# Kernel tuning notes

Hardware: AMD Instinct MI355X
Metric: run time of the kernel (lower is better)

Reference implementation:

```python
import jax, jax.numpy as jnp
import numpy as np

N_NODES = 100000
N_EDGES = 800000
IN_DIM, HID_DIM, OUT_DIM = 128, 256, 128


def setup_inputs() -> dict:
    key = jax.random.key(0)
    ks = jax.random.split(key, 8)
    x = jax.random.normal(ks[0], (N_NODES, IN_DIM), dtype=jnp.float32)
    edge_index = jax.random.randint(ks[1], (2, N_EDGES), 0, N_NODES, dtype=jnp.int32)
    s = lambda k, shp, fan_in: jax.random.normal(k, shp, dtype=jnp.float32) / np.sqrt(fan_in)
    return {
        "x": x,
        "edge_index": edge_index,
        "W1_l": s(ks[2], (HID_DIM, IN_DIM), IN_DIM),   # applied to aggregated neighbors
        "b1": jnp.zeros((HID_DIM,), jnp.float32),
        "W1_r": s(ks[3], (HID_DIM, IN_DIM), IN_DIM),   # root/self transform (no bias, as in PyG)
        "W2_l": s(ks[4], (OUT_DIM, HID_DIM), HID_DIM),
        "b2": jnp.zeros((OUT_DIM,), jnp.float32),
        "W2_r": s(ks[5], (OUT_DIM, HID_DIM), HID_DIM),
    }


def _sage_conv(x, src, dst, W_l, b, W_r):
    # mean aggregation of source-neighbor features onto targets
    msg = x[src]                                              # [E, d]
    agg = jax.ops.segment_sum(msg, dst, num_segments=N_NODES)  # [N, d]
    cnt = jax.ops.segment_sum(jnp.ones((src.shape[0],), x.dtype), dst, num_segments=N_NODES)
    mean = agg / jnp.maximum(cnt, 1.0)[:, None]
    # SAGEConv: lin_l(aggr) + lin_r(x)
    return mean @ W_l.T + b + x @ W_r.T


def reference(x, edge_index, W1_l, b1, W1_r, W2_l, b2, W2_r):
    src, dst = edge_index[0], edge_index[1]
    h = jax.nn.relu(_sage_conv(x, src, dst, W1_l, b1, W1_r))
    # dropout p=0.0 -> identity (eval-mode equivalent)
    out = _sage_conv(h, src, dst, W2_l, b2, W2_r)
    return out
```

## Files before the change

### kernel.cpp

```cpp
#include <hip/hip_runtime.h>

#define NN 100000
#define NE 800000

typedef __attribute__((ext_vector_type(4))) float f32x4;
typedef __attribute__((ext_vector_type(4))) int   i32x4;
typedef __attribute__((ext_vector_type(8))) unsigned short u16x8;

__device__ __forceinline__ unsigned short f2bf(float f) {
  unsigned u = __float_as_uint(f);
  return (unsigned short)((u + 0x7FFFu + ((u >> 16) & 1u)) >> 16);
}
__device__ __forceinline__ float bf2f(unsigned short b) {
  return __uint_as_float(((unsigned)b) << 16);
}

__global__ void degree_k(const int* __restrict__ dst, int* __restrict__ deg,
                         int* __restrict__ rord) {
  int e = blockIdx.x * 256 + threadIdx.x;
  if (e < NE) rord[e] = atomicAdd(&deg[dst[e]], 1);
}

__global__ __launch_bounds__(256) void scan1_k(const int* __restrict__ deg,
    int* __restrict__ offs, int* __restrict__ bsum, float* __restrict__ inv) {
  __shared__ int s[256];
  int t = threadIdx.x;
  int base = blockIdx.x * 1024 + t * 4;
  int v[4], tsum = 0;
#pragma unroll
  for (int k = 0; k < 4; ++k) {
    int i = base + k;
    v[k] = (i < NN) ? deg[i] : 0;
    tsum += v[k];
    if (i < NN) inv[i] = 1.0f / fmaxf((float)v[k], 1.0f);
  }
  s[t] = tsum; __syncthreads();
  int val = tsum;
#pragma unroll
  for (int off = 1; off < 256; off <<= 1) {
    int x = (t >= off) ? s[t - off] : 0;
    __syncthreads();
    val += x; s[t] = val;
    __syncthreads();
  }
  int excl = val - tsum;
  if (t == 255) bsum[blockIdx.x] = val;
  int run = excl;
#pragma unroll
  for (int k = 0; k < 4; ++k) { int i = base + k; if (i < NN) offs[i] = run; run += v[k]; }
}

__global__ __launch_bounds__(256) void scan2_k(int* __restrict__ bsum, int nb) {
  __shared__ int s[256];
  int t = threadIdx.x;
  int v = (t < nb) ? bsum[t] : 0;
  s[t] = v; __syncthreads();
  int val = v;
#pragma unroll
  for (int off = 1; off < 256; off <<= 1) {
    int x = (t >= off) ? s[t - off] : 0;
    __syncthreads();
    val += x; s[t] = val;
    __syncthreads();
  }
  if (t < nb) bsum[t] = val - v;
}

__global__ __launch_bounds__(256) void scan3_k(int* __restrict__ offs,
    const int* __restrict__ bsum) {
  int base = blockIdx.x * 1024 + threadIdx.x * 4;
  int add = bsum[blockIdx.x];
#pragma unroll
  for (int k = 0; k < 4; ++k) {
    int i = base + k;
    if (i < NN) offs[i] += add;
  }
}

__global__ void fill_k(const int* __restrict__ src, const int* __restrict__ dst,
    const int* __restrict__ offs, const int* __restrict__ rord,
    int* __restrict__ eidx) {
  int e = blockIdx.x * 256 + threadIdx.x;
  if (e < NE) {
    int p = offs[dst[e]] + rord[e];
    __builtin_nontemporal_store(src[e], &eidx[p]);
  }
}

__global__ __launch_bounds__(256) void cast_x_k(const float* __restrict__ in,
    unsigned short* __restrict__ outb) {
  int i = blockIdx.x * 256 + threadIdx.x;
  if (i >= NN * 128 / 4) return;
  float4 v = *reinterpret_cast<const float4*>(in + (size_t)i * 4);
  ushort4 o;
  o.x = f2bf(v.x); o.y = f2bf(v.y); o.z = f2bf(v.z); o.w = f2bf(v.w);
  *reinterpret_cast<ushort4*>(outb + (size_t)i * 4) = o;
}

__global__ __launch_bounds__(256) void cast_w4_k(const float* __restrict__ Wa,
    const float* __restrict__ Wb, const float* __restrict__ Wc,
    const float* __restrict__ Wd, unsigned short* __restrict__ outb) {
  int i = blockIdx.x * 256 + threadIdx.x;
  if (i >= 4 * 32768) return;
  int seg = i >> 15, off = i & 32767;
  const float* s = (seg < 2) ? (seg == 0 ? Wa : Wb) : (seg == 2 ? Wc : Wd);
  outb[i] = f2bf(s[off]);
}

template<bool ACC>
__global__ __launch_bounds__(256) void gather_k(const unsigned short* __restrict__ feat,
    const int* __restrict__ offs, const int* __restrict__ deg,
    const float* __restrict__ inv, const int* __restrict__ eidx,
    unsigned short* __restrict__ outb, float* __restrict__ outf) {
  int node = blockIdx.x * 16 + (threadIdx.x >> 4);
  int l = threadIdx.x & 15;
  if (node >= NN) return;
  int st = offs[node], n = deg[node];
  float a[8];
#pragma unroll
  for (int k = 0; k < 8; ++k) a[k] = 0.f;

  int j = 0;
  for (; j + 4 <= n; j += 4) {
    int s0 = eidx[st + j + 0];
    int s1 = eidx[st + j + 1];
    int s2 = eidx[st + j + 2];
    int s3 = eidx[st + j + 3];
    u16x8 r0 = *reinterpret_cast<const u16x8*>(feat + (size_t)s0 * 128 + l * 8);
    u16x8 r1 = *reinterpret_cast<const u16x8*>(feat + (size_t)s1 * 128 + l * 8);
    u16x8 r2 = *reinterpret_cast<const u16x8*>(feat + (size_t)s2 * 128 + l * 8);
    u16x8 r3 = *reinterpret_cast<const u16x8*>(feat + (size_t)s3 * 128 + l * 8);
#pragma unroll
    for (int k = 0; k < 8; ++k)
      a[k] += (bf2f(r0[k]) + bf2f(r1[k])) + (bf2f(r2[k]) + bf2f(r3[k]));
  }
  for (; j < n; ++j) {
    int s = eidx[st + j];
    u16x8 r = *reinterpret_cast<const u16x8*>(feat + (size_t)s * 128 + l * 8);
#pragma unroll
    for (int k = 0; k < 8; ++k) a[k] += bf2f(r[k]);
  }

  float sc = inv[node];
  if (ACC) {
    float* po = outf + (size_t)node * 128 + l * 8;
    float4 o0 = *reinterpret_cast<const float4*>(po);
    float4 o1 = *reinterpret_cast<const float4*>(po + 4);
    o0.x += sc * a[0]; o0.y += sc * a[1]; o0.z += sc * a[2]; o0.w += sc * a[3];
    o1.x += sc * a[4]; o1.y += sc * a[5]; o1.z += sc * a[6]; o1.w += sc * a[7];
    *reinterpret_cast<float4*>(po) = o0;
    *reinterpret_cast<float4*>(po + 4) = o1;
  } else {
    u16x8 o;
#pragma unroll
    for (int k = 0; k < 8; ++k) o[k] = f2bf(sc * a[k]);
    *reinterpret_cast<u16x8*>(outb + (size_t)node * 128 + l * 8) = o;
  }
}

template<int MODE>
__global__ __launch_bounds__(256) void mgemm_k(
    const unsigned short* __restrict__ A1, const unsigned short* __restrict__ A2,
    const unsigned short* __restrict__ Wbase, const float* __restrict__ bias,
    unsigned short* __restrict__ outb, float* __restrict__ outf) {
  __shared__ unsigned short As[64 * 256];
  const int t = threadIdx.x;
  const int wave = t >> 6, lane = t & 63;
  const int lhi = lane >> 4, llo = lane & 15;
  const int row0 = blockIdx.x * 64;

#pragma unroll
  for (int c = 0; c < 8; ++c) {
    int chunk = wave * 8 + c;
    int tb = chunk * 1024 + lane * 16;
    int r = tb >> 9;
    int cb = tb & 511;
    int cbs = cb ^ ((r & 7) << 4);
    int gr = min(row0 + r, NN - 1);
    const char* gsrc;
    if (MODE == 0) {
      const unsigned short* Asel = (cbs < 256) ? A1 : A2;
      gsrc = (const char*)(Asel + (size_t)gr * 128) + (cbs & 255);
    } else {
      gsrc = (const char*)(A1 + (size_t)gr * 256) + cbs;
    }
    __builtin_amdgcn_global_load_lds(
        (const __attribute__((address_space(1))) void*)gsrc,
        (__attribute__((address_space(3))) void*)((char*)As + chunk * 1024),
        16, 0, 0);
  }

  const unsigned short* bp[4];
  float bv[4];
#pragma unroll
  for (int fn = 0; fn < 4; ++fn) {
    int c = wave * 64 + fn * 16 + llo;
    if (MODE == 0) {
      bp[fn] = Wbase + (size_t)c * 128;
      bv[fn] = bias[c];
    } else {
      bp[fn] = Wbase + (wave >= 2 ? 32768 : 0) + (size_t)(c & 127) * 256;
      bv[fn] = (wave >= 2) ? bias[c & 127] : 0.f;
    }
  }

  f32x4 acc[4][4];
#pragma unroll
  for (int fm = 0; fm < 4; ++fm)
#pragma unroll
    for (int fn = 0; fn < 4; ++fn) acc[fm][fn] = (f32x4)0.f;

  __syncthreads();

#pragma unroll 1
  for (int ks = 0; ks < 8; ++ks) {
    i32x4 a[4], b[4];
#pragma unroll
    for (int fm = 0; fm < 4; ++fm) {
      int r = fm * 16 + llo;
      int cb = (ks * 64 + lhi * 16) ^ ((r & 7) << 4);
      a[fm] = *reinterpret_cast<const i32x4*>((const char*)As + r * 512 + cb);
    }
    int koff = (MODE == 0) ? ((ks & 3) * 32 + lhi * 8 + ((ks >= 4) ? 32768 : 0))
                           : (ks * 32 + lhi * 8);
#pragma unroll
    for (int fn = 0; fn < 4; ++fn)
      b[fn] = *reinterpret_cast<const i32x4*>(bp[fn] + koff);
#pragma unroll
    for (int fm = 0; fm < 4; ++fm)
#pragma unroll
      for (int fn = 0; fn < 4; ++fn)
        asm("v_mfma_f32_16x16x32_bf16 %0, %1, %2, %0"
            : "+v"(acc[fm][fn]) : "v"(a[fm]), "v"(b[fn]));
  }

  asm volatile("s_nop 7\n\ts_nop 7");

#pragma unroll
  for (int fm = 0; fm < 4; ++fm) {
#pragma unroll
    for (int fn = 0; fn < 4; ++fn) {
      int col = wave * 64 + fn * 16 + llo;
#pragma unroll
      for (int j = 0; j < 4; ++j) {
        int row = row0 + fm * 16 + lhi * 4 + j;
        if (row < NN) {
          float v = acc[fm][fn][j] + bv[fn];
          if (MODE == 0) {
            v = fmaxf(v, 0.f);
            outb[(size_t)row * 256 + col] = f2bf(v);
          } else if (wave < 2) {
            outb[(size_t)row * 128 + col] = f2bf(v);
          } else {
            outf[(size_t)row * 128 + (col - 128)] = v;
          }
        }
      }
    }
  }
}

extern "C" void kernel_launch(void* const* d_in, const int* in_sizes, int n_in,
                              void* d_out, int out_size, void* d_ws, size_t ws_size,
                              hipStream_t stream) {
  const float* x   = (const float*)d_in[0];
  const int*   ei  = (const int*)d_in[1];
  const float* W1l = (const float*)d_in[2];
  const float* b1  = (const float*)d_in[3];
  const float* W1r = (const float*)d_in[4];
  const float* W2l = (const float*)d_in[5];
  const float* b2  = (const float*)d_in[6];
  const float* W2r = (const float*)d_in[7];
  float* out = (float*)d_out;

  char* ws = (char*)d_ws;
  float*          inv    = (float*)(ws);
  int*            deg    = (int*)(ws + 0x80000);
  int*            offs   = (int*)(ws + 0x100000);
  int*            bsum   = (int*)(ws + 0x200000);
  unsigned short* Wb     = (unsigned short*)(ws + 0x280000);
  int*            eidx   = (int*)(ws + 0x400000);
  unsigned short* xb     = (unsigned short*)(ws + 0x800000);
  unsigned short* m1b    = (unsigned short*)(ws + 0x2200000);
  unsigned short* hb     = (unsigned short*)(ws + 0x3C00000);
  unsigned short* hWb    = (unsigned short*)(ws + 0x6E00000);
  int*            rord   = (int*)(ws + 0x8600000);

  const int* src = ei;
  const int* dst = ei + NE;
  const int NB = (NN + 1023) / 1024;

  hipMemsetAsync(deg, 0, NN * sizeof(int), stream);
  degree_k<<<(NE + 255) / 256, 256, 0, stream>>>(dst, deg, rord);
  scan1_k<<<NB, 256, 0, stream>>>(deg, offs, bsum, inv);
  scan2_k<<<1, 256, 0, stream>>>(bsum, NB);
  scan3_k<<<NB, 256, 0, stream>>>(offs, bsum);
  fill_k<<<(NE + 255) / 256, 256, 0, stream>>>(src, dst, offs, rord, eidx);

  cast_x_k<<<(NN * 128 / 4 + 255) / 256, 256, 0, stream>>>(x, xb);
  cast_w4_k<<<(4 * 32768 + 255) / 256, 256, 0, stream>>>(W1l, W1r, W2l, W2r, Wb);

  const int GB = (NN + 63) / 64;

  gather_k<false><<<(NN + 15) / 16, 256, 0, stream>>>(xb, offs, deg, inv, eidx, m1b, nullptr);
  mgemm_k<0><<<GB, 256, 0, stream>>>(m1b, xb, Wb, b1, hb, nullptr);

  mgemm_k<1><<<GB, 256, 0, stream>>>(hb, nullptr, Wb + 65536, b2, hWb, out);
  gather_k<true><<<(NN + 15) / 16, 256, 0, stream>>>(hWb, offs, deg, inv, eidx, nullptr, out);
}
```

Before: 249.9 us.

## Make GEMMs persistent with double-buffered LDS and register-resident weights

```diff
diff --git a/kernel.cpp b/kernel.cpp
--- a/kernel.cpp
+++ b/kernel.cpp
@@ -107,10 +107,11 @@
   outb[i] = f2bf(s[off]);
 }
 
-template<bool ACC>
+template<int GMODE>
 __global__ __launch_bounds__(256) void gather_k(const unsigned short* __restrict__ feat,
     const int* __restrict__ offs, const int* __restrict__ deg,
     const float* __restrict__ inv, const int* __restrict__ eidx,
+    const unsigned short* __restrict__ selfb,
     unsigned short* __restrict__ outb, float* __restrict__ outf) {
   int node = blockIdx.x * 16 + (threadIdx.x >> 4);
   int l = threadIdx.x & 15;
@@ -142,12 +143,14 @@
   }
 
   float sc = inv[node];
-  if (ACC) {
+  if (GMODE == 2) {
+    u16x8 sb = *reinterpret_cast<const u16x8*>(selfb + (size_t)node * 128 + l * 8);
+    float4 o0, o1;
+    o0.x = bf2f(sb[0]) + sc * a[0]; o0.y = bf2f(sb[1]) + sc * a[1];
+    o0.z = bf2f(sb[2]) + sc * a[2]; o0.w = bf2f(sb[3]) + sc * a[3];
+    o1.x = bf2f(sb[4]) + sc * a[4]; o1.y = bf2f(sb[5]) + sc * a[5];
+    o1.z = bf2f(sb[6]) + sc * a[6]; o1.w = bf2f(sb[7]) + sc * a[7];
     float* po = outf + (size_t)node * 128 + l * 8;
-    float4 o0 = *reinterpret_cast<const float4*>(po);
-    float4 o1 = *reinterpret_cast<const float4*>(po + 4);
-    o0.x += sc * a[0]; o0.y += sc * a[1]; o0.z += sc * a[2]; o0.w += sc * a[3];
-    o1.x += sc * a[4]; o1.y += sc * a[5]; o1.z += sc * a[6]; o1.w += sc * a[7];
     *reinterpret_cast<float4*>(po) = o0;
     *reinterpret_cast<float4*>(po + 4) = o1;
   } else {
@@ -159,104 +162,121 @@
 }
 
 template<int MODE>
-__global__ __launch_bounds__(256) void mgemm_k(
+__global__ __launch_bounds__(256, 2) void mgemm_k(
     const unsigned short* __restrict__ A1, const unsigned short* __restrict__ A2,
     const unsigned short* __restrict__ Wbase, const float* __restrict__ bias,
-    unsigned short* __restrict__ outb, float* __restrict__ outf) {
-  __shared__ unsigned short As[64 * 256];
+    unsigned short* __restrict__ outb, unsigned short* __restrict__ outb2) {
+  __shared__ unsigned short As[2][64 * 256];
   const int t = threadIdx.x;
   const int wave = t >> 6, lane = t & 63;
   const int lhi = lane >> 4, llo = lane & 15;
-  const int row0 = blockIdx.x * 64;
-
-#pragma unroll
-  for (int c = 0; c < 8; ++c) {
-    int chunk = wave * 8 + c;
-    int tb = chunk * 1024 + lane * 16;
-    int r = tb >> 9;
-    int cb = tb & 511;
-    int cbs = cb ^ ((r & 7) << 4);
-    int gr = min(row0 + r, NN - 1);
-    const char* gsrc;
-    if (MODE == 0) {
-      const unsigned short* Asel = (cbs < 256) ? A1 : A2;
-      gsrc = (const char*)(Asel + (size_t)gr * 128) + (cbs & 255);
-    } else {
-      gsrc = (const char*)(A1 + (size_t)gr * 256) + cbs;
-    }
-    __builtin_amdgcn_global_load_lds(
-        (const __attribute__((address_space(1))) void*)gsrc,
-        (__attribute__((address_space(3))) void*)((char*)As + chunk * 1024),
-        16, 0, 0);
-  }
-
-  const unsigned short* bp[4];
+
+  i32x4 bfrag[8][4];
   float bv[4];
 #pragma unroll
   for (int fn = 0; fn < 4; ++fn) {
     int c = wave * 64 + fn * 16 + llo;
+    const unsigned short* rowp;
     if (MODE == 0) {
-      bp[fn] = Wbase + (size_t)c * 128;
+      rowp = Wbase + (size_t)c * 128;
       bv[fn] = bias[c];
     } else {
-      bp[fn] = Wbase + (wave >= 2 ? 32768 : 0) + (size_t)(c & 127) * 256;
+      rowp = Wbase + (wave >= 2 ? 32768 : 0) + (size_t)(c & 127) * 256;
       bv[fn] = (wave >= 2) ? bias[c & 127] : 0.f;
     }
-  }
-
-  f32x4 acc[4][4];
-#pragma unroll
-  for (int fm = 0; fm < 4; ++fm)
-#pragma unroll
-    for (int fn = 0; fn < 4; ++fn) acc[fm][fn] = (f32x4)0.f;
-
-  __syncthreads();
+#pragma unroll
+    for (int ks = 0; ks < 8; ++ks) {
+      int koff = (MODE == 0) ? ((ks & 3) * 32 + lhi * 8 + ((ks >= 4) ? 32768 : 0))
+                             : (ks * 32 + lhi * 8);
+      bfrag[ks][fn] = *reinterpret_cast<const i32x4*>(rowp + koff);
+    }
+  }
+
+  auto stage = [&](int buf, int row0) {
+#pragma unroll
+    for (int c = 0; c < 8; ++c) {
+      int chunk = wave * 8 + c;
+      int tb = chunk * 1024 + lane * 16;
+      int r = tb >> 9;
+      int cb = tb & 511;
+      int cbs = cb ^ ((r & 7) << 4);
+      int gr = min(row0 + r, NN - 1);
+      const char* gsrc;
+      if (MODE == 0) {
+        const unsigned short* Asel = (cbs < 256) ? A1 : A2;
+        gsrc = (const char*)(Asel + (size_t)gr * 128) + (cbs & 255);
+      } else {
+        gsrc = (const char*)(A1 + (size_t)gr * 256) + cbs;
+      }
+      __builtin_amdgcn_global_load_lds(
+          (const __attribute__((address_space(1))) void*)gsrc,
+          (__attribute__((address_space(3))) void*)((char*)As + buf * 32768 + chunk * 1024),
+          16, 0, 0);
+    }
+  };
+
+  const int npan = (NN + 63) >> 6;
+  int p = blockIdx.x;
+  stage(0, p * 64);
+  int cur = 0;
 
 #pragma unroll 1
-  for (int ks = 0; ks < 8; ++ks) {
-    i32x4 a[4], b[4];
+  for (; p < npan; p += gridDim.x) {
+    int pn = p + gridDim.x;
+    if (pn < npan) stage(cur ^ 1, pn * 64);
+    asm volatile("s_waitcnt vmcnt(8)" ::: "memory");
+    __builtin_amdgcn_s_barrier();
+
+    const int row0 = p * 64;
+    f32x4 acc[4][4];
+#pragma unroll
+    for (int fm = 0; fm < 4; ++fm)
+#pragma unroll
+      for (int fn = 0; fn < 4; ++fn) acc[fm][fn] = (f32x4)0.f;
+
+#pragma unroll
+    for (int ks = 0; ks < 8; ++ks) {
+      i32x4 a[4];
+#pragma unroll
+      for (int fm = 0; fm < 4; ++fm) {
+        int r = fm * 16 + llo;
+        int cb = (ks * 64 + lhi * 16) ^ ((r & 7) << 4);
+        a[fm] = *reinterpret_cast<const i32x4*>((const char*)As + cur * 32768 + r * 512 + cb);
+      }
+#pragma unroll
+      for (int fm = 0; fm < 4; ++fm)
+#pragma unroll
+        for (int fn = 0; fn < 4; ++fn)
+          asm("v_mfma_f32_16x16x32_bf16 %0, %1, %2, %0"
+              : "+v"(acc[fm][fn]) : "v"(a[fm]), "v"(bfrag[ks][fn]));
+    }
+
+    asm volatile("s_nop 7\n\ts_nop 7");
+
 #pragma unroll
     for (int fm = 0; fm < 4; ++fm) {
-      int r = fm * 16 + llo;
-      int cb = (ks * 64 + lhi * 16) ^ ((r & 7) << 4);
-      a[fm] = *reinterpret_cast<const i32x4*>((const char*)As + r * 512 + cb);
-    }
-    int koff = (MODE == 0) ? ((ks & 3) * 32 + lhi * 8 + ((ks >= 4) ? 32768 : 0))
-                           : (ks * 32 + lhi * 8);
-#pragma unroll
-    for (int fn = 0; fn < 4; ++fn)
-      b[fn] = *reinterpret_cast<const i32x4*>(bp[fn] + koff);
-#pragma unroll
-    for (int fm = 0; fm < 4; ++fm)
-#pragma unroll
-      for (int fn = 0; fn < 4; ++fn)
-        asm("v_mfma_f32_16x16x32_bf16 %0, %1, %2, %0"
-            : "+v"(acc[fm][fn]) : "v"(a[fm]), "v"(b[fn]));
-  }
-
-  asm volatile("s_nop 7\n\ts_nop 7");
-
-#pragma unroll
-  for (int fm = 0; fm < 4; ++fm) {
-#pragma unroll
-    for (int fn = 0; fn < 4; ++fn) {
-      int col = wave * 64 + fn * 16 + llo;
-#pragma unroll
-      for (int j = 0; j < 4; ++j) {
-        int row = row0 + fm * 16 + lhi * 4 + j;
-        if (row < NN) {
-          float v = acc[fm][fn][j] + bv[fn];
-          if (MODE == 0) {
-            v = fmaxf(v, 0.f);
-            outb[(size_t)row * 256 + col] = f2bf(v);
-          } else if (wave < 2) {
-            outb[(size_t)row * 128 + col] = f2bf(v);
-          } else {
-            outf[(size_t)row * 128 + (col - 128)] = v;
+#pragma unroll
+      for (int fn = 0; fn < 4; ++fn) {
+        int col = wave * 64 + fn * 16 + llo;
+#pragma unroll
+        for (int j = 0; j < 4; ++j) {
+          int row = row0 + fm * 16 + lhi * 4 + j;
+          if (row < NN) {
+            float v = acc[fm][fn][j] + bv[fn];
+            if (MODE == 0) {
+              v = fmaxf(v, 0.f);
+              outb[(size_t)row * 256 + col] = f2bf(v);
+            } else if (wave < 2) {
+              outb[(size_t)row * 128 + col] = f2bf(v);
+            } else {
+              outb2[(size_t)row * 128 + (col - 128)] = f2bf(v);
+            }
           }
         }
       }
     }
+    __builtin_amdgcn_s_barrier();
+    cur ^= 1;
   }
 }
 
@@ -285,6 +305,7 @@
   unsigned short* hb     = (unsigned short*)(ws + 0x3C00000);
   unsigned short* hWb    = (unsigned short*)(ws + 0x6E00000);
   int*            rord   = (int*)(ws + 0x8600000);
+  unsigned short* selfb  = m1b;
 
   const int* src = ei;
   const int* dst = ei + NE;
@@ -300,11 +321,9 @@
   cast_x_k<<<(NN * 128 / 4 + 255) / 256, 256, 0, stream>>>(x, xb);
   cast_w4_k<<<(4 * 32768 + 255) / 256, 256, 0, stream>>>(W1l, W1r, W2l, W2r, Wb);
 
-  const int GB = (NN + 63) / 64;
-
-  gather_k<false><<<(NN + 15) / 16, 256, 0, stream>>>(xb, offs, deg, inv, eidx, m1b, nullptr);
-  mgemm_k<0><<<GB, 256, 0, stream>>>(m1b, xb, Wb, b1, hb, nullptr);
-
-  mgemm_k<1><<<GB, 256, 0, stream>>>(hb, nullptr, Wb + 65536, b2, hWb, out);
-  gather_k<true><<<(NN + 15) / 16, 256, 0, stream>>>(hWb, offs, deg, inv, eidx, nullptr, out);
-}
+  gather_k<0><<<(NN + 15) / 16, 256, 0, stream>>>(xb, offs, deg, inv, eidx, nullptr, m1b, nullptr);
+  mgemm_k<0><<<512, 256, 0, stream>>>(m1b, xb, Wb, b1, hb, nullptr);
+
+  mgemm_k<1><<<512, 256, 0, stream>>>(hb, nullptr, Wb + 65536, b2, hWb, selfb);
+  gather_k<2><<<(NN + 15) / 16, 256, 0, stream>>>(hWb, offs, deg, inv, eidx, selfb, nullptr, out);
+}
```

After: 226.3 us. -9.5%, faster.
